# Performance work log

Measured on AMD Instinct MI355X. Metric: run time of the kernel, lower is better.

## Reference

```python
import jax, jax.numpy as jnp
import numpy as np

MARGIN = 0.5


def _pairwise_sq_dists(x):
    # [N, N] squared euclidean distances
    sq = jnp.sum(x * x, axis=-1)  # [N]
    d = sq[:, None] + sq[None, :] - 2.0 * (x @ x.T)
    return jnp.maximum(d, 0.0)


def setup_inputs() -> dict:
    key = jax.random.key(0)
    k1, k2 = jax.random.split(key)
    N, D, NUM_CLASSES = 8192, 64, 128
    embeddings = jax.random.normal(k1, (N, D), dtype=jnp.float32)
    targets = jax.random.randint(k2, (N,), 0, NUM_CLASSES, dtype=jnp.int64)
    return {"embeddings": embeddings, "targets": targets}


def reference(embeddings, targets):
    # Batch-hard online triplet mining (vectorized form of the CPU loop):
    # for each anchor i: hard positive = argmax dist over same-class,
    # hard negative = argmin dist over other-class.
    dist = _pairwise_sq_dists(embeddings)  # [N, N]
    same = targets[:, None] == targets[None, :]  # [N, N] bool
    hard_pos = jnp.argmax(jnp.where(same, dist, -jnp.inf), axis=1)  # [N]
    hard_neg = jnp.argmin(jnp.where(same, jnp.inf, dist), axis=1)  # [N]
    # Recompute squared distances from embeddings for the selected triplets
    ap = jnp.sum(jnp.square(embeddings - embeddings[hard_pos]), axis=1)  # [N]
    an = jnp.sum(jnp.square(embeddings - embeddings[hard_neg]), axis=1)  # [N]
    losses = jax.nn.relu(ap - an + MARGIN)
    return jnp.mean(losses)
```

## Files before the change

### kernel.cpp

```cpp
#include <hip/hip_runtime.h>
#include <stdint.h>

#define N 8192
#define Dq 64
#define SPLITS 16
#define MARGIN 0.5f

typedef __attribute__((ext_vector_type(8))) short short8;
typedef __attribute__((ext_vector_type(16))) float floatx16;

__device__ __forceinline__ unsigned short f2bf(float f) {
  unsigned u = __float_as_uint(f);
  u += 0x7FFF + ((u >> 16) & 1);
  return (unsigned short)(u >> 16);
}

__global__ __launch_bounds__(256) void prep_kernel(
    const float* __restrict__ emb,
    unsigned short* __restrict__ embB, unsigned short* __restrict__ sqb,
    unsigned* __restrict__ pmax, unsigned* __restrict__ pmin,
    float* __restrict__ out) {
  int tid = blockIdx.x * 256 + threadIdx.x;
  int row = tid >> 4;
  int c = tid & 15;
  float4 v = reinterpret_cast<const float4*>(emb)[row * 16 + c];
  float s = v.x * v.x + v.y * v.y + v.z * v.z + v.w * v.w;
  #pragma unroll
  for (int off = 1; off < 16; off <<= 1) s += __shfl_xor(s, off);
  if (c == 0) sqb[row] = f2bf(-(0.5f * s + 2.0f));
  ushort4 b;
  b.x = f2bf(v.x); b.y = f2bf(v.y); b.z = f2bf(v.z); b.w = f2bf(v.w);
  reinterpret_cast<ushort4*>(embB)[row * 16 + c] = b;
  if (tid < N) { pmax[tid] = 0u; pmin[tid] = 0xFFFFFFFFu; }
  if (tid == 0) out[0] = 0.f;
}

__global__ __launch_bounds__(256, 4) void mine_kernel(
    const unsigned short* __restrict__ embB,
    const unsigned short* __restrict__ sqb, const int* __restrict__ cls,
    unsigned* __restrict__ pmax, unsigned* __restrict__ pmin) {
  const int lane = threadIdx.x & 63;
  const int wave = threadIdx.x >> 6;
  const int lo = lane & 31;
  const int half = lane >> 5;
  const int rowBase = (blockIdx.x * 4 + wave) * 32;
  const int tBase = blockIdx.y * (256 / SPLITS);

  const short8* ea =
      reinterpret_cast<const short8*>(embB + (size_t)(rowBase + lo) * Dq + half * 8);
  short8 a0 = ea[0], a1 = ea[2], a2 = ea[4], a3 = ea[6];
  unsigned short sqm = sqb[rowBase + lo];
  const short one = (short)0x3F80;
  short8 a4 = {(short)(half == 0 ? one : 0),
               (short)(half == 0 ? (short)sqm : 0), 0, 0, 0, 0, 0, 0};

  int ci[16];
  #pragma unroll
  for (int r = 0; r < 16; ++r)
    ci[r] = cls[rowBase + (r & 3) + 8 * (r >> 2) + 4 * half];

  unsigned maxk[16], mink[16];
  #pragma unroll
  for (int r = 0; r < 16; ++r) { maxk[r] = 0u; mink[r] = 0xFFFFFFFFu; }

  #pragma unroll 2
  for (int t = 0; t < 256 / SPLITS; ++t) {
    const int cb = (tBase + t) * 32;
    const short8* eb =
        reinterpret_cast<const short8*>(embB + (size_t)(cb + lo) * Dq + half * 8);
    short8 b0 = eb[0], b1 = eb[2], b2 = eb[4], b3 = eb[6];
    unsigned short sqn = sqb[cb + lo];
    int cj = cls[cb + lo];
    short8 b4 = {(short)(half == 0 ? (short)sqn : 0),
                 (short)(half == 0 ? one : 0), 0, 0, 0, 0, 0, 0};

    floatx16 acc;
    #pragma unroll
    for (int i = 0; i < 16; ++i) acc[i] = 0.f;
    acc = __builtin_amdgcn_mfma_f32_32x32x16_bf16(a0, b0, acc, 0, 0, 0);
    acc = __builtin_amdgcn_mfma_f32_32x32x16_bf16(a1, b1, acc, 0, 0, 0);
    acc = __builtin_amdgcn_mfma_f32_32x32x16_bf16(a2, b2, acc, 0, 0, 0);
    acc = __builtin_amdgcn_mfma_f32_32x32x16_bf16(a3, b3, acc, 0, 0, 0);
    acc = __builtin_amdgcn_mfma_f32_32x32x16_bf16(a4, b4, acc, 0, 0, 0);

    const unsigned j = cb + lo;
    const unsigned jinv = 8191u - j;
    #pragma unroll
    for (int r = 0; r < 16; ++r) {
      unsigned kb = __float_as_uint(acc[r]) & 0xFFFFE000u;
      bool same = (ci[r] == cj);
      unsigned kp = same ? (kb | jinv) : 0u;
      unsigned kn = same ? 0xFFFFFFFFu : (kb | j);
      maxk[r] = maxk[r] > kp ? maxk[r] : kp;
      mink[r] = mink[r] < kn ? mink[r] : kn;
    }
  }

  #pragma unroll
  for (int off = 1; off < 32; off <<= 1) {
    #pragma unroll
    for (int r = 0; r < 16; ++r) {
      unsigned om = (unsigned)__shfl_xor((int)maxk[r], off);
      maxk[r] = maxk[r] > om ? maxk[r] : om;
      unsigned on = (unsigned)__shfl_xor((int)mink[r], off);
      mink[r] = mink[r] < on ? mink[r] : on;
    }
  }

  if (lo == 0) {
    #pragma unroll
    for (int r = 0; r < 16; ++r) {
      int row = rowBase + (r & 3) + 8 * (r >> 2) + 4 * half;
      atomicMax(&pmax[row], maxk[r]);
      atomicMin(&pmin[row], mink[r]);
    }
  }
}

__global__ __launch_bounds__(256) void finalize_kernel(
    const float* __restrict__ emb,
    const unsigned* __restrict__ pmax, const unsigned* __restrict__ pmin,
    float* __restrict__ out) {
  int tid = blockIdx.x * 256 + threadIdx.x;
  int anchor = tid >> 2;
  int part = tid & 3;
  int jp = 8191 - (int)(pmax[anchor] & 8191u);
  int jn = (int)(pmin[anchor] & 8191u);

  const float4* xi = reinterpret_cast<const float4*>(emb + (size_t)anchor * Dq) + part * 4;
  const float4* xp = reinterpret_cast<const float4*>(emb + (size_t)jp * Dq) + part * 4;
  const float4* xn = reinterpret_cast<const float4*>(emb + (size_t)jn * Dq) + part * 4;
  float ap = 0.f, an = 0.f;
  #pragma unroll
  for (int k = 0; k < 4; ++k) {
    float4 a = xi[k], p = xp[k], q = xn[k];
    float dx = a.x - p.x, dy = a.y - p.y, dz = a.z - p.z, dw = a.w - p.w;
    ap += dx * dx + dy * dy + dz * dz + dw * dw;
    dx = a.x - q.x; dy = a.y - q.y; dz = a.z - q.z; dw = a.w - q.w;
    an += dx * dx + dy * dy + dz * dz + dw * dw;
  }
  #pragma unroll
  for (int off = 1; off < 4; off <<= 1) {
    ap += __shfl_xor(ap, off);
    an += __shfl_xor(an, off);
  }
  float loss = (part == 0) ? fmaxf(ap - an + MARGIN, 0.f) : 0.f;
  #pragma unroll
  for (int off = 4; off < 64; off <<= 1) loss += __shfl_xor(loss, off);
  __shared__ float wsum[4];
  if ((threadIdx.x & 63) == 0) wsum[threadIdx.x >> 6] = loss;
  __syncthreads();
  if (threadIdx.x == 0)
    atomicAdd(out, (wsum[0] + wsum[1] + wsum[2] + wsum[3]) * (1.0f / (float)N));
}

extern "C" void kernel_launch(void* const* d_in, const int* in_sizes, int n_in,
                              void* d_out, int out_size, void* d_ws, size_t ws_size,
                              hipStream_t stream) {
  const float* emb = (const float*)d_in[0];
  const int* tgt = (const int*)d_in[1];
  float* out = (float*)d_out;

  char* ws = (char*)d_ws;
  unsigned short* embB = (unsigned short*)ws;
  unsigned short* sqb = (unsigned short*)(ws + (size_t)N * Dq * 2);
  unsigned* pmax = (unsigned*)(ws + (size_t)N * Dq * 2 + N * 2);
  unsigned* pmin = pmax + N;

  prep_kernel<<<N * 16 / 256, 256, 0, stream>>>(emb, embB, sqb, pmax, pmin, out);
  mine_kernel<<<dim3(N / 128, SPLITS), 256, 0, stream>>>(embB, sqb, tgt, pmax, pmin);
  finalize_kernel<<<N * 4 / 256, 256, 0, stream>>>(emb, pmax, pmin, out);
}
```

Before: 99.63 us.

## Store bf16 embeddings in MFMA fragment order for coalesced operand loads

The prep kernel now writes the bf16 embeddings in a tiled layout where each 32-row tile's MFMA operand fragments sit contiguously per lane. The mining kernel can then load each fragment with fully coalesced 16-byte loads instead of strided row-major loads. The zero accumulator is also hoisted out of the loop. One side effect is that the prep grid is halved, because each thread now converts 8 elements. The risk is a layout indexing mistake, though the layout appears consistent with the lane mapping used before.

```diff
diff --git a/kernel.cpp b/kernel.cpp
--- a/kernel.cpp
+++ b/kernel.cpp
@@ -17,38 +17,46 @@
 
 __global__ __launch_bounds__(256) void prep_kernel(
     const float* __restrict__ emb,
-    unsigned short* __restrict__ embB, unsigned short* __restrict__ sqb,
+    unsigned short* __restrict__ embF, unsigned short* __restrict__ sqb,
     unsigned* __restrict__ pmax, unsigned* __restrict__ pmin,
     float* __restrict__ out) {
   int tid = blockIdx.x * 256 + threadIdx.x;
-  int row = tid >> 4;
-  int c = tid & 15;
-  float4 v = reinterpret_cast<const float4*>(emb)[row * 16 + c];
-  float s = v.x * v.x + v.y * v.y + v.z * v.z + v.w * v.w;
+  int row = tid >> 3;
+  int m = tid & 7;
+  const float4* src = reinterpret_cast<const float4*>(emb) + (size_t)row * 16 + m * 2;
+  float4 v0 = src[0], v1 = src[1];
+  float s = v0.x * v0.x + v0.y * v0.y + v0.z * v0.z + v0.w * v0.w
+          + v1.x * v1.x + v1.y * v1.y + v1.z * v1.z + v1.w * v1.w;
   #pragma unroll
-  for (int off = 1; off < 16; off <<= 1) s += __shfl_xor(s, off);
-  if (c == 0) sqb[row] = f2bf(-(0.5f * s + 2.0f));
-  ushort4 b;
-  b.x = f2bf(v.x); b.y = f2bf(v.y); b.z = f2bf(v.z); b.w = f2bf(v.w);
-  reinterpret_cast<ushort4*>(embB)[row * 16 + c] = b;
+  for (int off = 1; off < 8; off <<= 1) s += __shfl_xor(s, off);
+  if (m == 0) sqb[row] = f2bf(-(0.5f * s + 2.0f));
+  short8 b;
+  b[0] = (short)f2bf(v0.x); b[1] = (short)f2bf(v0.y);
+  b[2] = (short)f2bf(v0.z); b[3] = (short)f2bf(v0.w);
+  b[4] = (short)f2bf(v1.x); b[5] = (short)f2bf(v1.y);
+  b[6] = (short)f2bf(v1.z); b[7] = (short)f2bf(v1.w);
+  size_t dst = (size_t)(row >> 5) * 2048 + (size_t)(m >> 1) * 512
+             + (size_t)((m & 1) * 32 + (row & 31)) * 8;
+  *reinterpret_cast<short8*>(embF + dst) = b;
   if (tid < N) { pmax[tid] = 0u; pmin[tid] = 0xFFFFFFFFu; }
   if (tid == 0) out[0] = 0.f;
 }
 
 __global__ __launch_bounds__(256, 4) void mine_kernel(
-    const unsigned short* __restrict__ embB,
+    const unsigned short* __restrict__ embF,
     const unsigned short* __restrict__ sqb, const int* __restrict__ cls,
     unsigned* __restrict__ pmax, unsigned* __restrict__ pmin) {
   const int lane = threadIdx.x & 63;
   const int wave = threadIdx.x >> 6;
   const int lo = lane & 31;
   const int half = lane >> 5;
-  const int rowBase = (blockIdx.x * 4 + wave) * 32;
+  const int aT = blockIdx.x * 4 + wave;
+  const int rowBase = aT * 32;
   const int tBase = blockIdx.y * (256 / SPLITS);
 
-  const short8* ea =
-      reinterpret_cast<const short8*>(embB + (size_t)(rowBase + lo) * Dq + half * 8);
-  short8 a0 = ea[0], a1 = ea[2], a2 = ea[4], a3 = ea[6];
+  const short8* fr = reinterpret_cast<const short8*>(embF);
+  const short8* ea = fr + (size_t)aT * 256 + lane;
+  short8 a0 = ea[0], a1 = ea[64], a2 = ea[128], a3 = ea[192];
   unsigned short sqm = sqb[rowBase + lo];
   const short one = (short)0x3F80;
   short8 a4 = {(short)(half == 0 ? one : 0),
@@ -59,25 +67,25 @@
   for (int r = 0; r < 16; ++r)
     ci[r] = cls[rowBase + (r & 3) + 8 * (r >> 2) + 4 * half];
 
+  floatx16 zacc;
+  #pragma unroll
+  for (int i = 0; i < 16; ++i) zacc[i] = 0.f;
+
   unsigned maxk[16], mink[16];
   #pragma unroll
   for (int r = 0; r < 16; ++r) { maxk[r] = 0u; mink[r] = 0xFFFFFFFFu; }
 
   #pragma unroll 2
-  for (int t = 0; t < 256 / SPLITS; ++t) {
-    const int cb = (tBase + t) * 32;
-    const short8* eb =
-        reinterpret_cast<const short8*>(embB + (size_t)(cb + lo) * Dq + half * 8);
-    short8 b0 = eb[0], b1 = eb[2], b2 = eb[4], b3 = eb[6];
+  for (int t = tBase; t < tBase + 256 / SPLITS; ++t) {
+    const int cb = t * 32;
+    const short8* eb = fr + (size_t)t * 256 + lane;
+    short8 b0 = eb[0], b1 = eb[64], b2 = eb[128], b3 = eb[192];
     unsigned short sqn = sqb[cb + lo];
     int cj = cls[cb + lo];
     short8 b4 = {(short)(half == 0 ? (short)sqn : 0),
                  (short)(half == 0 ? one : 0), 0, 0, 0, 0, 0, 0};
 
-    floatx16 acc;
-    #pragma unroll
-    for (int i = 0; i < 16; ++i) acc[i] = 0.f;
-    acc = __builtin_amdgcn_mfma_f32_32x32x16_bf16(a0, b0, acc, 0, 0, 0);
+    floatx16 acc = __builtin_amdgcn_mfma_f32_32x32x16_bf16(a0, b0, zacc, 0, 0, 0);
     acc = __builtin_amdgcn_mfma_f32_32x32x16_bf16(a1, b1, acc, 0, 0, 0);
     acc = __builtin_amdgcn_mfma_f32_32x32x16_bf16(a2, b2, acc, 0, 0, 0);
     acc = __builtin_amdgcn_mfma_f32_32x32x16_bf16(a3, b3, acc, 0, 0, 0);
@@ -162,12 +170,12 @@
   float* out = (float*)d_out;
 
   char* ws = (char*)d_ws;
-  unsigned short* embB = (unsigned short*)ws;
+  unsigned short* embF = (unsigned short*)ws;
   unsigned short* sqb = (unsigned short*)(ws + (size_t)N * Dq * 2);
   unsigned* pmax = (unsigned*)(ws + (size_t)N * Dq * 2 + N * 2);
   unsigned* pmin = pmax + N;
 
-  prep_kernel<<<N * 16 / 256, 256, 0, stream>>>(emb, embB, sqb, pmax, pmin, out);
-  mine_kernel<<<dim3(N / 128, SPLITS), 256, 0, stream>>>(embB, sqb, tgt, pmax, pmin);
+  prep_kernel<<<N * 8 / 256, 256, 0, stream>>>(emb, embF, sqb, pmax, pmin, out);
+  mine_kernel<<<dim3(N / 128, SPLITS), 256, 0, stream>>>(embF, sqb, tgt, pmax, pmin);
   finalize_kernel<<<N * 4 / 256, 256, 0, stream>>>(emb, pmax, pmin, out);
 }
```

Measured after the change: 90.93 us. -8.7%, faster.
